# Optimization experiments

Hardware: AMD Instinct MI355X
Metric: run time of the kernel (lower is better)

The kernel has to match this reference:

```python
import jax, jax.numpy as jnp
import numpy as np

INPUT, HIDDEN, OUTPUT = 512, 1024, 512


def setup_inputs() -> dict:
    key = jax.random.key(0)
    k1, k2, k3, k4, k5 = jax.random.split(key, 5)
    fan = INPUT + HIDDEN
    s = 1.0 / np.sqrt(fan)
    so = 1.0 / np.sqrt(HIDDEN)
    return {
        "x": jax.random.normal(k1, (64, 512, INPUT), dtype=jnp.float32),
        "W": jax.random.uniform(k2, (fan, 4 * HIDDEN), jnp.float32, -s, s),
        "b": jax.random.uniform(k3, (4 * HIDDEN,), jnp.float32, -s, s),
        "W_out": jax.random.uniform(k4, (HIDDEN, OUTPUT), jnp.float32, -so, so),
        "b_out": jax.random.uniform(k5, (OUTPUT,), jnp.float32, -so, so),
    }


def reference(x, W, b, W_out, b_out):
    B, T, _ = x.shape
    h = HIDDEN
    h0 = jnp.zeros((B, h), dtype=x.dtype)
    c0 = jnp.zeros((B, h), dtype=x.dtype)

    def step(carry, xt):
        hs, cs = carry
        # fused gate pre-activation: [B, 4h]
        f = jnp.concatenate([xt, hs], axis=1) @ W + b
        fg = jax.nn.sigmoid(f[:, :h])          # forget gate
        ig = jax.nn.sigmoid(f[:, h:2 * h])     # input gate
        gg = jnp.tanh(f[:, 2 * h:3 * h])       # candidate
        og = jax.nn.sigmoid(f[:, 3 * h:])      # output gate
        cs = cs * fg + ig * gg
        hs = og * jnp.tanh(cs)
        return (hs, cs), None

    (hT, _), _ = jax.lax.scan(step, (h0, c0), jnp.swapaxes(x, 0, 1))
    return hT @ W_out + b_out
```

## Files before the change

kernel.cpp:

```cpp
#include <hip/hip_runtime.h>


#define B_   64
#define T_   512
#define IN_  512
#define H_   1024
#define G4_  4096
#define OUT_ 512

typedef _Float16 f16;
typedef _Float16 f16x8 __attribute__((ext_vector_type(8)));
typedef _Float16 f16x4 __attribute__((ext_vector_type(4)));
typedef float f32x4  __attribute__((ext_vector_type(4)));
typedef float f32x16 __attribute__((ext_vector_type(16)));

#define X16_OFF   0UL
#define WOT_OFF   33554432UL
#define H_OFF     (WOT_OFF + 1048576UL)
#define FLG_OFF   (H_OFF + 262144UL)
#define WS_NEED   (FLG_OFF + 4096UL)
#define ZERO_BYTES (262144UL + 4096UL)

__device__ __forceinline__ float sigmoidf_(float v) { return 1.f / (1.f + __expf(-v)); }
__device__ __forceinline__ float tanhf_(float v) { return 1.f - 2.f / (__expf(2.f * v) + 1.f); }

__device__ __forceinline__ f16x8 ld_agent_b128(const f16* p) {
  f16x8 r;
  asm volatile("global_load_dwordx4 %0, %1, off sc0 sc1" : "=v"(r) : "v"(p));
  return r;
}
__device__ __forceinline__ void at_swap_b32(unsigned* p, unsigned v) {
  asm volatile("global_atomic_swap %0, %1, off sc1" :: "v"(p), "v"(v) : "memory");
}
__device__ __forceinline__ unsigned ld_flag(const unsigned* p) {
  unsigned r;
  asm volatile("global_load_dword %0, %1, off sc0 sc1" : "=v"(r) : "v"(p));
  return r;
}
__device__ __forceinline__ void wait_vm0() {
  asm volatile("s_waitcnt vmcnt(0)" ::: "memory");
  __builtin_amdgcn_sched_barrier(0);
}
__device__ __forceinline__ void wait_vm1() {
  asm volatile("s_waitcnt vmcnt(1)" ::: "memory");
  __builtin_amdgcn_sched_barrier(0);
}

__global__ __launch_bounds__(256) void lstm_prepass(
    const float* __restrict__ x, const float* __restrict__ Wout,
    f16* __restrict__ x16, f16* __restrict__ WoT) {
  long i = (long)blockIdx.x * blockDim.x + threadIdx.x;
  long stride = (long)gridDim.x * blockDim.x;
  const long n4 = (long)B_ * T_ * IN_ / 4;
  const float4* x4 = (const float4*)x;
  f16x4* o4 = (f16x4*)x16;
  for (long p = i; p < n4; p += stride) {
    float4 v = x4[p];
    f16x4 o = { (f16)v.x, (f16)v.y, (f16)v.z, (f16)v.w };
    o4[p] = o;
  }
  const long nw = (long)H_ * OUT_;
  for (long p = i; p < nw; p += stride) {
    long k = p / OUT_, c = p % OUT_;
    WoT[c * (long)H_ + k] = (f16)Wout[p];
  }
}

__global__ __launch_bounds__(512, 2) void lstm_main(
    const float* __restrict__ W, const float* __restrict__ b,
    const f16* __restrict__ x16, f16* hbuf, unsigned* flags) {

  const int wg   = blockIdx.x;
  const int g    = wg >> 6;
  const int wgi  = wg & 63;
  const int tid  = threadIdx.x;
  const int wave = tid >> 6;
  const int lane = tid & 63;

  const int hbase   = wgi * 16;
  const int colLane = lane & 31;
  const int khalf   = (lane >> 5) * 8;
  const int arow    = lane & 31;

  f16x8 wf[24];
  #pragma unroll
  for (int n = 0; n < 2; ++n) {
    const int gate = n * 2 + (colLane >> 4);
    const int gcol = gate * H_ + hbase + (colLane & 15);
    #pragma unroll
    for (int kf = 0; kf < 12; ++kf) {
      const int k0 = (kf < 4) ? (64 * wave + 16 * kf)
                              : (512 + 128 * wave + 16 * (kf - 4));
      f16x8 v;
      #pragma unroll
      for (int j = 0; j < 8; ++j)
        v[j] = (f16)W[(long)(k0 + khalf + j) * G4_ + gcol];
      wf[n * 12 + kf] = v;
    }
  }

  const int erow = tid >> 4;
  const int ej   = tid & 15;
  float bias[4];
  #pragma unroll
  for (int gt = 0; gt < 4; ++gt) bias[gt] = b[gt * H_ + hbase + ej];

  float c_state = 0.f;

  __shared__ float red[2][8][32][68];

  const f16* xg = x16 + (long)(g * 32) * T_ * IN_;
  f16* hb       = hbuf + (long)g * 2 * 32 * H_;
  unsigned* flg = flags + g * 64 * 8;

  const unsigned* fp = flg + 64 * wave + lane;
  unsigned* myflag = flg + wgi * 8 + wave;

  f32x16 acc0 = {}, acc1 = {};
  {
    const f16* xrow = xg + (long)arow * (T_ * IN_) + 64 * wave + khalf;
    f16x8 xa[4];
    #pragma unroll
    for (int f = 0; f < 4; ++f) xa[f] = *(const f16x8*)(xrow + 16 * f);
    #pragma unroll
    for (int kf = 0; kf < 4; ++kf) {
      acc0 = __builtin_amdgcn_mfma_f32_32x32x16_f16(xa[kf], wf[kf],      acc0, 0, 0, 0);
      acc1 = __builtin_amdgcn_mfma_f32_32x32x16_f16(xa[kf], wf[12 + kf], acc1, 0, 0, 0);
    }
  }

  for (int t = 0; t < T_; ++t) {
    const int buf = t & 1;

    if (t > 0) {
      const unsigned tgt = (unsigned)t;
      int guard = 0;
      unsigned v0 = ld_flag(fp);
      unsigned v1 = 0;
      for (;;) {
        v1 = ld_flag(fp);
        wait_vm1();
        if (__all(v0 >= tgt) || ++guard > (1 << 22)) break;
        v0 = ld_flag(fp);
        wait_vm1();
        if (__all(v1 >= tgt) || ++guard > (1 << 22)) break;
      }
      asm volatile("s_waitcnt vmcnt(0)" ::: "memory");
      asm volatile("" :: "v"(v0), "v"(v1));
      __builtin_amdgcn_sched_barrier(0);
    }

    {
      const f16* hrow = hb + (long)buf * (32 * H_) + (long)arow * H_
                           + 128 * wave + khalf;
      f16x8 ha[8];
      #pragma unroll
      for (int f = 0; f < 8; ++f)
        ha[f] = ld_agent_b128(hrow + 16 * f);
      wait_vm0();
      #pragma unroll
      for (int kf = 0; kf < 8; ++kf) {
        acc0 = __builtin_amdgcn_mfma_f32_32x32x16_f16(ha[kf], wf[4 + kf],  acc0, 0, 0, 0);
        acc1 = __builtin_amdgcn_mfma_f32_32x32x16_f16(ha[kf], wf[16 + kf], acc1, 0, 0, 0);
      }
    }

    {
      float (*rb)[32][68] = red[buf];
      #pragma unroll
      for (int r = 0; r < 16; ++r) {
        const int row = (r & 3) + 8 * (r >> 2) + 4 * (lane >> 5);
        rb[wave][row][colLane]      = acc0[r];
        rb[wave][row][32 + colLane] = acc1[r];
      }
    }
    __syncthreads();

    {
      const float (*rb)[32][68] = red[buf];
      float f4[4];
      #pragma unroll
      for (int gt = 0; gt < 4; ++gt) {
        float s = bias[gt];
        #pragma unroll
        for (int w = 0; w < 8; ++w) s += rb[w][erow][gt * 16 + ej];
        f4[gt] = s;
      }
      const float fg = sigmoidf_(f4[0]);
      const float ig = sigmoidf_(f4[1]);
      const float gg = tanhf_(f4[2]);
      const float og = sigmoidf_(f4[3]);
      c_state = c_state * fg + ig * gg;
      const float hv = og * tanhf_(c_state);

      const unsigned h16 =
          (unsigned)__builtin_bit_cast(unsigned short, (f16)hv);
      const unsigned hi = (unsigned)__shfl_xor((int)h16, 1, 64);
      if ((lane & 1) == 0) {
        unsigned pk = h16 | (hi << 16);
        unsigned* p = (unsigned*)&hb[(long)(buf ^ 1) * (32 * H_)
                                     + (long)erow * H_ + hbase + ej];
        at_swap_b32(p, pk);
      }
      wait_vm0();
      if (lane == 0)
        at_swap_b32(myflag, (unsigned)(t + 1));
    }

    acc0 = f32x16{}; acc1 = f32x16{};
    if (t + 1 < T_) {
      const f16* xrow = xg + (long)arow * (T_ * IN_) + (long)(t + 1) * IN_
                           + 64 * wave + khalf;
      f16x8 xa[4];
      #pragma unroll
      for (int f = 0; f < 4; ++f) xa[f] = *(const f16x8*)(xrow + 16 * f);
      #pragma unroll
      for (int kf = 0; kf < 4; ++kf) {
        acc0 = __builtin_amdgcn_mfma_f32_32x32x16_f16(xa[kf], wf[kf],      acc0, 0, 0, 0);
        acc1 = __builtin_amdgcn_mfma_f32_32x32x16_f16(xa[kf], wf[12 + kf], acc1, 0, 0, 0);
      }
    }
  }
}

__global__ __launch_bounds__(256) void lstm_out(
    const f16* __restrict__ hbuf, const f16* __restrict__ WoT,
    const float* __restrict__ bout, float* __restrict__ out) {
  const int wgid = blockIdx.x;
  const int rowT = wgid >> 5;
  const int colT = wgid & 31;
  const int tid  = threadIdx.x;
  const int wave = tid >> 6;
  const int lane = tid & 63;
  const int r16  = lane & 15;
  const int ksel = (lane >> 4) * 8;

  const int g = rowT >> 1;
  const f16* hrow = hbuf + (long)g * 2 * 32 * H_
                  + (long)((rowT & 1) * 16 + r16) * H_;
  const f16* wrow = WoT + (long)(colT * 16 + r16) * H_;

  f32x4 acc = {};
  #pragma unroll
  for (int f = 0; f < 8; ++f) {
    f16x8 a  = *(const f16x8*)(hrow + 256 * wave + 32 * f + ksel);
    f16x8 bf = *(const f16x8*)(wrow + 256 * wave + 32 * f + ksel);
    acc = __builtin_amdgcn_mfma_f32_16x16x32_f16(a, bf, acc, 0, 0, 0);
  }

  __shared__ float red[4][16][20];
  #pragma unroll
  for (int r = 0; r < 4; ++r)
    red[wave][(lane >> 4) * 4 + r][lane & 15] = acc[r];
  __syncthreads();

  const int row = tid >> 4;
  const int col = tid & 15;
  float s = bout[colT * 16 + col];
  #pragma unroll
  for (int w = 0; w < 4; ++w) s += red[w][row][col];
  out[(long)(rowT * 16 + row) * OUT_ + colT * 16 + col] = s;
}

extern "C" void kernel_launch(void* const* d_in, const int* in_sizes, int n_in,
                              void* d_out, int out_size, void* d_ws, size_t ws_size,
                              hipStream_t stream) {
  const float* x    = (const float*)d_in[0];
  const float* W    = (const float*)d_in[1];
  const float* b    = (const float*)d_in[2];
  const float* Wout = (const float*)d_in[3];
  const float* bout = (const float*)d_in[4];
  float* out = (float*)d_out;

  if (ws_size < WS_NEED) return;

  char* wsb = (char*)d_ws;
  f16* x16  = (f16*)(wsb + X16_OFF);
  f16* WoT  = (f16*)(wsb + WOT_OFF);
  f16* hbuf = (f16*)(wsb + H_OFF);
  unsigned* flags = (unsigned*)(wsb + FLG_OFF);

  hipMemsetAsync(wsb + H_OFF, 0, ZERO_BYTES, stream);

  lstm_prepass<<<1024, 256, 0, stream>>>(x, Wout, x16, WoT);

  lstm_main<<<128, 512, 0, stream>>>(W, b, x16, hbuf, flags);

  lstm_out<<<128, 256, 0, stream>>>(hbuf, WoT, bout, out);
}
```

Baseline: 2.439 ms.

## Use per-timestep hidden-state buffers with cached loads and plain agent stores

When the workspace is large enough, each timestep writes its hidden state to its own slot in a 513-slot history buffer instead of double-buffering. Because no address is ever rewritten, the recurrent h reads can use ordinary cached loads instead of system-coherent ones. The h and flag publications switch from atomic swaps to plain agent-scope stores. The fallback path for a small workspace also launches an extra 2048-step unsynchronized lstm_main into scratch buffers before the real run; this looks like a warm-up or probe and adds work. The cached loads rely on stale cache lines never being present for the fresh slots.

```diff
diff --git a/kernel.cpp b/kernel.cpp
--- a/kernel.cpp
+++ b/kernel.cpp
@@ -16,10 +16,14 @@
 
 #define X16_OFF   0UL
 #define WOT_OFF   33554432UL
-#define H_OFF     (WOT_OFF + 1048576UL)
-#define FLG_OFF   (H_OFF + 262144UL)
-#define WS_NEED   (FLG_OFF + 4096UL)
-#define ZERO_BYTES (262144UL + 4096UL)
+#define HS_OFF    34603008UL
+#define FLG_OFF   34865152UL
+#define HSCR_OFF  34869248UL
+#define FSCR_OFF  35131392UL
+#define WS_SMALL  35135488UL
+#define HBIG_OFF  35135488UL
+#define HBIG_BYTES (513UL * 2 * 32 * 1024 * 2)
+#define WS_BIG    (HBIG_OFF + HBIG_BYTES)
 
 __device__ __forceinline__ float sigmoidf_(float v) { return 1.f / (1.f + __expf(-v)); }
 __device__ __forceinline__ float tanhf_(float v) { return 1.f - 2.f / (__expf(2.f * v) + 1.f); }
@@ -29,8 +33,13 @@
   asm volatile("global_load_dwordx4 %0, %1, off sc0 sc1" : "=v"(r) : "v"(p));
   return r;
 }
-__device__ __forceinline__ void at_swap_b32(unsigned* p, unsigned v) {
-  asm volatile("global_atomic_swap %0, %1, off sc1" :: "v"(p), "v"(v) : "memory");
+__device__ __forceinline__ f16x8 ld_cached_b128(const f16* p) {
+  f16x8 r;
+  asm volatile("global_load_dwordx4 %0, %1, off" : "=v"(r) : "v"(p));
+  return r;
+}
+__device__ __forceinline__ void st_agent_b32(unsigned* p, unsigned v) {
+  asm volatile("global_store_dword %0, %1, off sc0 sc1" :: "v"(p), "v"(v) : "memory");
 }
 __device__ __forceinline__ unsigned ld_flag(const unsigned* p) {
   unsigned r;
@@ -66,6 +75,7 @@
   }
 }
 
+template<int MODE, int TSTEPS, bool BIG>
 __global__ __launch_bounds__(512, 2) void lstm_main(
     const float* __restrict__ W, const float* __restrict__ b,
     const f16* __restrict__ x16, f16* hbuf, unsigned* flags) {
@@ -77,7 +87,7 @@
   const int wave = tid >> 6;
   const int lane = tid & 63;
 
-  const int hbase   = wgi * 16;
+  const int cbase   = wgi * 16;
   const int colLane = lane & 31;
   const int khalf   = (lane >> 5) * 8;
   const int arow    = lane & 31;
@@ -86,7 +96,7 @@
   #pragma unroll
   for (int n = 0; n < 2; ++n) {
     const int gate = n * 2 + (colLane >> 4);
-    const int gcol = gate * H_ + hbase + (colLane & 15);
+    const int gcol = gate * H_ + cbase + (colLane & 15);
     #pragma unroll
     for (int kf = 0; kf < 12; ++kf) {
       const int k0 = (kf < 4) ? (64 * wave + 16 * kf)
@@ -103,18 +113,26 @@
   const int ej   = tid & 15;
   float bias[4];
   #pragma unroll
-  for (int gt = 0; gt < 4; ++gt) bias[gt] = b[gt * H_ + hbase + ej];
+  for (int gt = 0; gt < 4; ++gt) bias[gt] = b[gt * H_ + cbase + ej];
 
   float c_state = 0.f;
 
   __shared__ float red[2][8][32][68];
 
   const f16* xg = x16 + (long)(g * 32) * T_ * IN_;
-  f16* hb       = hbuf + (long)g * 2 * 32 * H_;
   unsigned* flg = flags + g * 64 * 8;
 
   const unsigned* fp = flg + 64 * wave + lane;
   unsigned* myflag = flg + wgi * 8 + wave;
+
+  auto hrd = [&](int t) -> const f16* {
+    if constexpr (BIG) return hbuf + ((long)t * 2 + g) * (32 * H_);
+    else               return hbuf + ((long)g * 2 + (t & 1)) * (32 * H_);
+  };
+  auto hwr = [&](int t) -> f16* {
+    if constexpr (BIG) return hbuf + ((long)(t + 1) * 2 + g) * (32 * H_);
+    else               return hbuf + ((long)g * 2 + ((t + 1) & 1)) * (32 * H_);
+  };
 
   f32x16 acc0 = {}, acc1 = {};
   {
@@ -129,34 +147,34 @@
     }
   }
 
-  for (int t = 0; t < T_; ++t) {
-    const int buf = t & 1;
-
-    if (t > 0) {
-      const unsigned tgt = (unsigned)t;
-      int guard = 0;
-      unsigned v0 = ld_flag(fp);
-      unsigned v1 = 0;
-      for (;;) {
-        v1 = ld_flag(fp);
-        wait_vm1();
-        if (__all(v0 >= tgt) || ++guard > (1 << 22)) break;
-        v0 = ld_flag(fp);
-        wait_vm1();
-        if (__all(v1 >= tgt) || ++guard > (1 << 22)) break;
-      }
-      asm volatile("s_waitcnt vmcnt(0)" ::: "memory");
-      asm volatile("" :: "v"(v0), "v"(v1));
-      __builtin_amdgcn_sched_barrier(0);
+  for (int t = 0; t < TSTEPS; ++t) {
+    if constexpr (MODE >= 1) {
+      if (t > 0) {
+        const unsigned tgt = (unsigned)t;
+        int guard = 0;
+        unsigned v0 = ld_flag(fp);
+        unsigned v1 = 0;
+        for (;;) {
+          v1 = ld_flag(fp);
+          wait_vm1();
+          if (__all(v0 >= tgt) || ++guard > (1 << 22)) break;
+          v0 = ld_flag(fp);
+          wait_vm1();
+          if (__all(v1 >= tgt) || ++guard > (1 << 22)) break;
+        }
+        asm volatile("s_waitcnt vmcnt(0)" ::: "memory");
+        asm volatile("" :: "v"(v0), "v"(v1));
+        __builtin_amdgcn_sched_barrier(0);
+      }
     }
 
     {
-      const f16* hrow = hb + (long)buf * (32 * H_) + (long)arow * H_
-                           + 128 * wave + khalf;
+      const f16* hrow = hrd(t) + (long)arow * H_ + 128 * wave + khalf;
       f16x8 ha[8];
       #pragma unroll
       for (int f = 0; f < 8; ++f)
-        ha[f] = ld_agent_b128(hrow + 16 * f);
+        ha[f] = BIG ? ld_cached_b128(hrow + 16 * f)
+                    : ld_agent_b128(hrow + 16 * f);
       wait_vm0();
       #pragma unroll
       for (int kf = 0; kf < 8; ++kf) {
@@ -166,7 +184,7 @@
     }
 
     {
-      float (*rb)[32][68] = red[buf];
+      float (*rb)[32][68] = red[t & 1];
       #pragma unroll
       for (int r = 0; r < 16; ++r) {
         const int row = (r & 3) + 8 * (r >> 2) + 4 * (lane >> 5);
@@ -177,7 +195,7 @@
     __syncthreads();
 
     {
-      const float (*rb)[32][68] = red[buf];
+      const float (*rb)[32][68] = red[t & 1];
       float f4[4];
       #pragma unroll
       for (int gt = 0; gt < 4; ++gt) {
@@ -198,18 +216,18 @@
       const unsigned hi = (unsigned)__shfl_xor((int)h16, 1, 64);
       if ((lane & 1) == 0) {
         unsigned pk = h16 | (hi << 16);
-        unsigned* p = (unsigned*)&hb[(long)(buf ^ 1) * (32 * H_)
-                                     + (long)erow * H_ + hbase + ej];
-        at_swap_b32(p, pk);
-      }
-      wait_vm0();
+        unsigned* p = (unsigned*)(hwr(t) + (long)erow * H_ + cbase + ej);
+        st_agent_b32(p, pk);
+      }
+      if constexpr (MODE == 2) wait_vm0();
       if (lane == 0)
-        at_swap_b32(myflag, (unsigned)(t + 1));
+        st_agent_b32(myflag, (unsigned)(t + 1));
     }
 
     acc0 = f32x16{}; acc1 = f32x16{};
-    if (t + 1 < T_) {
-      const f16* xrow = xg + (long)arow * (T_ * IN_) + (long)(t + 1) * IN_
+    if (t + 1 < TSTEPS) {
+      const int tx = (t + 1) & (T_ - 1);
+      const f16* xrow = xg + (long)arow * (T_ * IN_) + (long)tx * IN_
                            + 64 * wave + khalf;
       f16x8 xa[4];
       #pragma unroll
@@ -224,7 +242,7 @@
 }
 
 __global__ __launch_bounds__(256) void lstm_out(
-    const f16* __restrict__ hbuf, const f16* __restrict__ WoT,
+    const f16* __restrict__ hT, long gs, const f16* __restrict__ WoT,
     const float* __restrict__ bout, float* __restrict__ out) {
   const int wgid = blockIdx.x;
   const int rowT = wgid >> 5;
@@ -236,8 +254,7 @@
   const int ksel = (lane >> 4) * 8;
 
   const int g = rowT >> 1;
-  const f16* hrow = hbuf + (long)g * 2 * 32 * H_
-                  + (long)((rowT & 1) * 16 + r16) * H_;
+  const f16* hrow = hT + (long)g * gs + (long)((rowT & 1) * 16 + r16) * H_;
   const f16* wrow = WoT + (long)(colT * 16 + r16) * H_;
 
   f32x4 acc = {};
@@ -272,19 +289,29 @@
   const float* bout = (const float*)d_in[4];
   float* out = (float*)d_out;
 
-  if (ws_size < WS_NEED) return;
+  if (ws_size < WS_SMALL) return;
 
   char* wsb = (char*)d_ws;
   f16* x16  = (f16*)(wsb + X16_OFF);
   f16* WoT  = (f16*)(wsb + WOT_OFF);
-  f16* hbuf = (f16*)(wsb + H_OFF);
   unsigned* flags = (unsigned*)(wsb + FLG_OFF);
 
-  hipMemsetAsync(wsb + H_OFF, 0, ZERO_BYTES, stream);
-
   lstm_prepass<<<1024, 256, 0, stream>>>(x, Wout, x16, WoT);
 
-  lstm_main<<<128, 512, 0, stream>>>(W, b, x16, hbuf, flags);
-
-  lstm_out<<<128, 256, 0, stream>>>(hbuf, WoT, bout, out);
-}
+  if (ws_size >= WS_BIG) {
+    f16* hbig = (f16*)(wsb + HBIG_OFF);
+    hipMemsetAsync(wsb + HBIG_OFF, 0, 2 * 32 * H_ * sizeof(f16), stream);
+    hipMemsetAsync(wsb + FLG_OFF, 0, 4096, stream);
+    lstm_main<2, 512, true><<<128, 512, 0, stream>>>(W, b, x16, hbig, flags);
+    lstm_out<<<128, 256, 0, stream>>>(hbig + (long)T_ * 2 * 32 * H_,
+                                      (long)32 * H_, WoT, bout, out);
+  } else {
+    f16* hsm  = (f16*)(wsb + HS_OFF);
+    f16* hscr = (f16*)(wsb + HSCR_OFF);
+    unsigned* fscr = (unsigned*)(wsb + FSCR_OFF);
+    hipMemsetAsync(wsb + HS_OFF, 0, WS_SMALL - HS_OFF, stream);
+    lstm_main<0, 2048, false><<<128, 512, 0, stream>>>(W, b, x16, hscr, fscr);
+    lstm_main<2, 512, false><<<128, 512, 0, stream>>>(W, b, x16, hsm, flags);
+    lstm_out<<<128, 256, 0, stream>>>(hsm, (long)2 * 32 * H_, WoT, bout, out);
+  }
+}
```

Result: faster. 2.312 ms (-5.2%).
